# Performance work log

Measured on AMD Instinct MI355X. Metric: run time of the kernel, lower is better.

## Reference

```python
import jax, jax.numpy as jnp
import numpy as np

DIM, HEADS, WS, SHIFT = 192, 6, 8, 4
EPS = 1e-5


def layer_norm(x, g, b):
    mu = jnp.mean(x, axis=-1, keepdims=True)
    var = jnp.mean(jnp.square(x - mu), axis=-1, keepdims=True)
    return (x - mu) * jax.lax.rsqrt(var + EPS) * g + b


def window_partition(x, ws):
    # x: [B, H, W, C] -> [B*nW, ws*ws, C]
    B, H, W, C = x.shape
    x = x.reshape(B, H // ws, ws, W // ws, ws, C)
    return x.transpose(0, 1, 3, 2, 4, 5).reshape(-1, ws * ws, C)


def window_merge(win, ws, B, H, W, C):
    x = win.reshape(B, H // ws, W // ws, ws, ws, C)
    return x.transpose(0, 1, 3, 2, 4, 5).reshape(B, H, W, C)


def make_shift_mask(H, W, ws, shift):
    # standard Swin attention mask for shifted windows (host-side constant)
    img = np.zeros((H, W), dtype=np.float32)
    cnt = 0
    slices = (slice(0, -ws), slice(-ws, -shift), slice(-shift, None))
    for hs in slices:
        for wsl in slices:
            img[hs, wsl] = cnt
            cnt += 1
    m = img.reshape(H // ws, ws, W // ws, ws).transpose(0, 2, 1, 3).reshape(-1, ws * ws)  # [nW, N]
    diff = m[:, None, :] - m[:, :, None]
    return jnp.asarray(np.where(diff != 0, -100.0, 0.0).astype(np.float32))  # [nW, N, N]


def swin_attention(x, qkv_w, qkv_b, proj_w, proj_b, shift):
    B, H, W, C = x.shape
    h, d = HEADS, C // HEADS
    scale = 1.0 / jnp.sqrt(jnp.asarray(d, x.dtype))
    if shift > 0:
        x = jnp.roll(x, shift=(-shift, -shift), axis=(1, 2))
    win = window_partition(x, WS)                       # [Bn, N, C]
    Bn, N, _ = win.shape
    qkv = win @ qkv_w + qkv_b                           # [Bn, N, 3C]
    qkv = qkv.reshape(Bn, N, 3, h, d).transpose(2, 0, 3, 1, 4)
    q, k, v = qkv[0], qkv[1], qkv[2]                    # [Bn, h, N, d]
    attn = jnp.einsum('bhnd,bhmd->bhnm', q, k) * scale  # [Bn, h, N, N]
    if shift > 0:
        mask = make_shift_mask(H, W, WS, shift)         # [nW, N, N]
        nW = mask.shape[0]
        attn = attn.reshape(Bn // nW, nW, h, N, N) + mask[None, :, None]
        attn = attn.reshape(Bn, h, N, N)
    attn = jax.nn.softmax(attn, axis=-1)
    out = jnp.einsum('bhnm,bhmd->bhnd', attn, v)        # [Bn, h, N, d]
    out = out.transpose(0, 2, 1, 3).reshape(Bn, N, C)
    out = out @ proj_w + proj_b
    out = window_merge(out, WS, B, H, W, C)
    if shift > 0:
        out = jnp.roll(out, shift=(shift, shift), axis=(1, 2))
    return out


def setup_inputs() -> dict:
    key = jax.random.key(0)
    ks = jax.random.split(key, 6)
    B, H, W, C = 8, 128, 128, DIM
    s = 0.02
    return {
        'x': jax.random.normal(ks[0], (B, H, W, C), jnp.float32),
        'ln1_g': jnp.ones((C,), jnp.float32),
        'ln1_b': jnp.zeros((C,), jnp.float32),
        'qkv1_w': jax.random.normal(ks[1], (C, 3 * C), jnp.float32) * s,
        'qkv1_b': jnp.zeros((3 * C,), jnp.float32),
        'proj1_w': jax.random.normal(ks[2], (C, C), jnp.float32) * s,
        'proj1_b': jnp.zeros((C,), jnp.float32),
        'ln2_g': jnp.ones((C,), jnp.float32),
        'ln2_b': jnp.zeros((C,), jnp.float32),
        'qkv2_w': jax.random.normal(ks[3], (C, 3 * C), jnp.float32) * s,
        'qkv2_b': jnp.zeros((3 * C,), jnp.float32),
        'proj2_w': jax.random.normal(ks[4], (C, C), jnp.float32) * s,
        'proj2_b': jnp.zeros((C,), jnp.float32),
    }


def reference(x, ln1_g, ln1_b, qkv1_w, qkv1_b, proj1_w, proj1_b,
              ln2_g, ln2_b, qkv2_w, qkv2_b, proj2_w, proj2_b):
    # W-MSA branch (mlp1 is an empty Sequential -> identity)
    y = layer_norm(x, ln1_g, ln1_b)
    x = x + swin_attention(y, qkv1_w, qkv1_b, proj1_w, proj1_b, shift=0)
    # SW-MSA branch (mlp2 is identity)
    y = layer_norm(x, ln2_g, ln2_b)
    x = x + swin_attention(y, qkv2_w, qkv2_b, proj2_w, proj2_b, shift=SHIFT)
    return x
```

## Files before the change

kernel.cpp:

```cpp
#include <hip/hip_runtime.h>

typedef unsigned int   u32;
typedef unsigned short u16;
typedef __bf16 bf16x8 __attribute__((ext_vector_type(8)));
typedef float  f32x4  __attribute__((ext_vector_type(4)));

__device__ __forceinline__ u16 f2bf(float f) {
    u32 u = __builtin_bit_cast(u32, f);
    u += 0x7FFFu + ((u >> 16) & 1u);
    return (u16)(u >> 16);
}
__device__ __forceinline__ u32 pk2bf(float a, float b) {
    return (u32)f2bf(a) | ((u32)f2bf(b) << 16);
}
__device__ __forceinline__ bf16x8 ldfrag(const u16* p) {
    return __builtin_bit_cast(bf16x8, *reinterpret_cast<const uint4*>(p));
}

__device__ __forceinline__ u32 swz(u32 i) { return i ^ ((i >> 3) & 7u); }

template<int SHIFT>
__global__ __launch_bounds__(768) void swin_branch(
    const float* __restrict__ xin, float* __restrict__ xout,
    const float* __restrict__ ln_g, const float* __restrict__ ln_b,
    const u16*   __restrict__ wqkv_t,
    const float* __restrict__ qkv_b,
    const u16*   __restrict__ wproj_t,
    const float* __restrict__ proj_b)
{
    __shared__ __align__(16) u16 smem[49152];
    __shared__ float red1[2][6][64];
    __shared__ float red2[2][6][64];
    constexpr u32 QOFF = 12288;

    const int tid  = threadIdx.x;
    const int win  = (tid >= 384) ? 1 : 0;
    const int lt   = tid - win*384;
    const int wid  = lt >> 6;
    const int lane = lt & 63;
    const int lr   = lane & 15;
    const int lg   = lane >> 4;
    const u32 lsw  = swz((u32)lane);
    const u32 SB   = (u32)win * 24576u;

    const int Wid = blockIdx.x*2 + win;
    const int b   = Wid >> 8;
    const int wy  = (Wid >> 4) & 15;
    const int wx  = Wid & 15;

    {
        const int ty = lane >> 3, tx = lane & 7;
        const int shy = (wy*8 + ty + SHIFT) & 127;
        const int shx = (wx*8 + tx + SHIFT) & 127;
        const float* xp = xin + ((size_t)((b*128 + shy)*128 + shx))*192 + wid*32;
        float xv[32];
        float s1 = 0.f, s2 = 0.f;
        #pragma unroll
        for (int j = 0; j < 8; ++j) {
            float4 v = reinterpret_cast<const float4*>(xp)[j];
            xv[j*4+0]=v.x; xv[j*4+1]=v.y; xv[j*4+2]=v.z; xv[j*4+3]=v.w;
            s1 += v.x+v.y+v.z+v.w;
            s2 += v.x*v.x + v.y*v.y + v.z*v.z + v.w*v.w;
        }
        red1[win][wid][lane] = s1; red2[win][wid][lane] = s2;
        __syncthreads();
        float a1 = 0.f, a2 = 0.f;
        #pragma unroll
        for (int w = 0; w < 6; ++w) { a1 += red1[win][w][lane]; a2 += red2[win][w][lane]; }
        const float mu = a1 * (1.f/192.f);
        const float rs = rsqrtf(a2 * (1.f/192.f) - mu*mu + 1e-5f);
        const float* gp = ln_g + wid*32;
        const float* bp = ln_b + wid*32;
        const u32 yblk = SB + (u32)((lg*6 + wid)*512);
        #pragma unroll
        for (int cc8 = 0; cc8 < 4; ++cc8) {
            u32 pk[4];
            #pragma unroll
            for (int q = 0; q < 4; ++q) {
                int j = cc8*8 + q*2;
                float y0 = (xv[j]   - mu)*rs*gp[j]   + bp[j];
                float y1 = (xv[j+1] - mu)*rs*gp[j+1] + bp[j+1];
                pk[q] = pk2bf(y0, y1);
            }
            *reinterpret_cast<uint4*>(&smem[yblk + swz((u32)(lr + 16*cc8))*8]) =
                make_uint4(pk[0],pk[1],pk[2],pk[3]);
        }
    }
    __syncthreads();

    uint2 kpk[4][2];
    uint2 vpk[4][2];
    {
        {
            f32x4 acc[4][4];
            #pragma unroll
            for (int mi=0; mi<4; ++mi)
                #pragma unroll
                for (int t=0; t<4; ++t) acc[mi][t] = f32x4{0.f,0.f,0.f,0.f};
            #pragma unroll
            for (int ks=0; ks<6; ++ks) {
                bf16x8 af[4];
                #pragma unroll
                for (int mi=0; mi<4; ++mi)
                    af[mi] = ldfrag(&smem[SB + (u32)((mi*6+ks)*512) + lsw*8]);
                bf16x8 bw[4];
                #pragma unroll
                for (int t=0; t<4; ++t)
                    bw[t] = ldfrag(&wqkv_t[((t>>1)*192 + wid*32 + (t&1)*16 + lr)*192 + 32*ks + 8*lg]);
                #pragma unroll
                for (int mi=0; mi<4; ++mi)
                    #pragma unroll
                    for (int t=0; t<4; ++t)
                        acc[mi][t] = __builtin_amdgcn_mfma_f32_16x16x32_bf16(af[mi], bw[t], acc[mi][t], 0,0,0);
            }
            #pragma unroll
            for (int t=0; t<2; ++t) {
                const float bias = qkv_b[wid*32 + t*16 + lr];
                const u32 lphi   = (u32)(16*(2*t + (lr>>3)));
                #pragma unroll
                for (int mi=0; mi<4; ++mi)
                    #pragma unroll
                    for (int rg=0; rg<4; ++rg) {
                        const u32 pos = (u32)(4*lg + rg) + lphi;
                        smem[SB + QOFF + (u32)(wid*2048) + mi*512 + swz(pos)*8 + (lr&7)] =
                            f2bf((acc[mi][t][rg] + bias) * 0.1767766952966369f);
                    }
            }
            #pragma unroll
            for (int t2=0; t2<2; ++t2) {
                const float bias = qkv_b[192 + wid*32 + t2*16 + lr];
                #pragma unroll
                for (int mi=0; mi<4; ++mi)
                    kpk[mi][t2] = make_uint2(
                        pk2bf(acc[mi][2+t2][0] + bias, acc[mi][2+t2][1] + bias),
                        pk2bf(acc[mi][2+t2][2] + bias, acc[mi][2+t2][3] + bias));
            }
        }
        {
            f32x4 vacc[4][2];
            #pragma unroll
            for (int mi=0; mi<4; ++mi)
                #pragma unroll
                for (int t=0; t<2; ++t) vacc[mi][t] = f32x4{0.f,0.f,0.f,0.f};
            #pragma unroll
            for (int ks=0; ks<6; ++ks) {
                bf16x8 af[4];
                #pragma unroll
                for (int mi=0; mi<4; ++mi)
                    af[mi] = ldfrag(&smem[SB + (u32)((mi*6+ks)*512) + lsw*8]);
                bf16x8 bw[2];
                #pragma unroll
                for (int t=0; t<2; ++t)
                    bw[t] = ldfrag(&wqkv_t[(384 + wid*32 + t*16 + lr)*192 + 32*ks + 8*lg]);
                #pragma unroll
                for (int mi=0; mi<4; ++mi)
                    #pragma unroll
                    for (int t=0; t<2; ++t)
                        vacc[mi][t] = __builtin_amdgcn_mfma_f32_16x16x32_bf16(af[mi], bw[t], vacc[mi][t], 0,0,0);
            }
            #pragma unroll
            for (int tv=0; tv<2; ++tv) {
                const float bias = qkv_b[384 + wid*32 + tv*16 + lr];
                #pragma unroll
                for (int mi=0; mi<4; ++mi)
                    vpk[mi][tv] = make_uint2(
                        pk2bf(vacc[mi][tv][0] + bias, vacc[mi][tv][1] + bias),
                        pk2bf(vacc[mi][tv][2] + bias, vacc[mi][tv][3] + bias));
            }
        }
    }
    __syncthreads();

    float rsum[4][4];
    f32x4 o_[4][2];
    {
        const u32 W  = SB + (u32)(wid*512);
        const u32 qb = SB + QOFF + (u32)(wid*2048);
        #define BLK(s) ((u32)(s)*3072u + W)

        #pragma unroll
        for (int t2=0; t2<2; ++t2) {
            const u32 lphi = (u32)(16*(2*t2 + (lr>>3)));
            #pragma unroll
            for (int mi=0; mi<4; ++mi) {
                const u32 a0 = BLK(mi) + (lr&7);
                smem[a0 + swz((u32)(4*lg+0) + lphi)*8] = (u16)(kpk[mi][t2].x);
                smem[a0 + swz((u32)(4*lg+1) + lphi)*8] = (u16)(kpk[mi][t2].x >> 16);
                smem[a0 + swz((u32)(4*lg+2) + lphi)*8] = (u16)(kpk[mi][t2].y);
                smem[a0 + swz((u32)(4*lg+3) + lphi)*8] = (u16)(kpk[mi][t2].y >> 16);
            }
        }
        bf16x8 aq[4], bk[4];
        #pragma unroll
        for (int mi=0; mi<4; ++mi) aq[mi] = ldfrag(&smem[qb + mi*512 + lsw*8]);
        #pragma unroll
        for (int ni=0; ni<4; ++ni) bk[ni] = ldfrag(&smem[BLK(ni) + lsw*8]);
        __builtin_amdgcn_sched_barrier(0);

        #pragma unroll
        for (int tv=0; tv<2; ++tv)
            #pragma unroll
            for (int mi=0; mi<4; ++mi) {
                const u32 pos = (u32)(lr + 16*(2*(mi&1) + (lg>>1)));
                *reinterpret_cast<uint2*>(
                    &smem[BLK(tv*2 + (mi>>1)) + swz(pos)*8 + 4*(lg&1)]) = vpk[mi][tv];
            }

        f32x4 s[4][4];
        #pragma unroll
        for (int mi=0; mi<4; ++mi)
            #pragma unroll
            for (int ni=0; ni<4; ++ni)
                s[mi][ni] = __builtin_amdgcn_mfma_f32_16x16x32_bf16(aq[mi], bk[ni],
                                f32x4{0.f,0.f,0.f,0.f}, 0,0,0);

        if constexpr (SHIFT > 0) {
            int kl[4];
            #pragma unroll
            for (int ni=0; ni<4; ++ni) {
                const int col = 16*ni + lr;
                const int hu = wy*8 + (col>>3);
                const int wu = wx*8 + (col&7);
                kl[ni] = ((hu >= 124) ? 2 : (hu >= 120 ? 1 : 0))*3
                       + ((wu >= 124) ? 2 : (wu >= 120 ? 1 : 0));
            }
            #pragma unroll
            for (int mi=0; mi<4; ++mi)
                #pragma unroll
                for (int rg=0; rg<4; ++rg) {
                    const int row = 16*mi + 4*lg + rg;
                    const int hu = wy*8 + (row>>3);
                    const int wu = wx*8 + (row&7);
                    const int rl = ((hu >= 124) ? 2 : (hu >= 120 ? 1 : 0))*3
                                 + ((wu >= 124) ? 2 : (wu >= 120 ? 1 : 0));
                    #pragma unroll
                    for (int ni=0; ni<4; ++ni)
                        if (rl != kl[ni]) s[mi][ni][rg] += -100.f;
                }
        }

        #pragma unroll
        for (int mi=0; mi<4; ++mi)
            #pragma unroll
            for (int rg=0; rg<4; ++rg) {
                float m = fmaxf(fmaxf(s[mi][0][rg], s[mi][1][rg]), fmaxf(s[mi][2][rg], s[mi][3][rg]));
                #pragma unroll
                for (int off=1; off<16; off<<=1) m = fmaxf(m, __shfl_xor(m, off, 64));
                float sm = 0.f;
                #pragma unroll
                for (int ni=0; ni<4; ++ni) {
                    float e = __expf(s[mi][ni][rg] - m);
                    s[mi][ni][rg] = e;
                    sm += e;
                }
                #pragma unroll
                for (int off=1; off<16; off<<=1) sm += __shfl_xor(sm, off, 64);
                rsum[mi][rg] = 1.0f / sm;
            }

        bf16x8 ap0[4], ap1[4];
        #pragma unroll
        for (int mi=0; mi<4; ++mi)
            #pragma unroll
            for (int ni=0; ni<2; ++ni)
                #pragma unroll
                for (int rg=0; rg<4; ++rg) {
                    const u32 pos = (u32)(4*lg + rg + 16*(2*ni + (lr>>3)));
                    smem[qb + mi*512 + swz(pos)*8 + (lr&7)] = f2bf(s[mi][ni][rg]);
                }
        #pragma unroll
        for (int mi=0; mi<4; ++mi) ap0[mi] = ldfrag(&smem[qb + mi*512 + lsw*8]);
        __builtin_amdgcn_sched_barrier(0);
        #pragma unroll
        for (int mi=0; mi<4; ++mi)
            #pragma unroll
            for (int ni=2; ni<4; ++ni)
                #pragma unroll
                for (int rg=0; rg<4; ++rg) {
                    const u32 pos = (u32)(4*lg + rg + 16*(2*(ni-2) + (lr>>3)));
                    smem[qb + mi*512 + swz(pos)*8 + (lr&7)] = f2bf(s[mi][ni][rg]);
                }
        #pragma unroll
        for (int mi=0; mi<4; ++mi) ap1[mi] = ldfrag(&smem[qb + mi*512 + lsw*8]);
        __builtin_amdgcn_sched_barrier(0);

        bf16x8 bv[2][2];
        #pragma unroll
        for (int tv=0; tv<2; ++tv)
            #pragma unroll
            for (int ksv=0; ksv<2; ++ksv)
                bv[tv][ksv] = ldfrag(&smem[BLK(tv*2+ksv) + lsw*8]);

        #pragma unroll
        for (int mi=0; mi<4; ++mi)
            #pragma unroll
            for (int tv=0; tv<2; ++tv) {
                o_[mi][tv] = __builtin_amdgcn_mfma_f32_16x16x32_bf16(ap0[mi], bv[tv][0],
                                 f32x4{0.f,0.f,0.f,0.f}, 0,0,0);
                o_[mi][tv] = __builtin_amdgcn_mfma_f32_16x16x32_bf16(ap1[mi], bv[tv][1],
                                 o_[mi][tv], 0,0,0);
            }
        __builtin_amdgcn_sched_barrier(0);

        #pragma unroll
        for (int mi=0; mi<4; ++mi)
            #pragma unroll
            for (int tv=0; tv<2; ++tv)
                #pragma unroll
                for (int rg=0; rg<4; ++rg) {
                    const u32 pos = (u32)(4*lg + rg + 16*(2*tv + (lr>>3)));
                    smem[BLK(mi) + swz(pos)*8 + (lr&7)] = f2bf(o_[mi][tv][rg] * rsum[mi][rg]);
                }
        #undef BLK
    }
    __syncthreads();

    {
        f32x4 a2[4][2];
        #pragma unroll
        for (int mi=0; mi<4; ++mi)
            #pragma unroll
            for (int ni=0; ni<2; ++ni) a2[mi][ni] = f32x4{0.f,0.f,0.f,0.f};
        #pragma unroll
        for (int ks=0; ks<6; ++ks) {
            bf16x8 af[4], bw[2];
            #pragma unroll
            for (int mi=0; mi<4; ++mi)
                af[mi] = ldfrag(&smem[SB + (u32)((mi*6+ks)*512) + lsw*8]);
            #pragma unroll
            for (int ni=0; ni<2; ++ni)
                bw[ni] = ldfrag(&wproj_t[(wid*32 + 16*ni + lr)*192 + 32*ks + 8*lg]);
            #pragma unroll
            for (int mi=0; mi<4; ++mi)
                #pragma unroll
                for (int ni=0; ni<2; ++ni)
                    a2[mi][ni] = __builtin_amdgcn_mfma_f32_16x16x32_bf16(af[mi], bw[ni], a2[mi][ni], 0,0,0);
        }
        #pragma unroll
        for (int ni=0; ni<2; ++ni) {
            const int c  = wid*32 + 16*ni + lr;
            const float pb = proj_b[c];
            #pragma unroll
            for (int mi=0; mi<4; ++mi)
                #pragma unroll
                for (int rg=0; rg<4; ++rg) {
                    const int row = 16*mi + 4*lg + rg;
                    const int ty = row >> 3, tx = row & 7;
                    const int shy = (wy*8 + ty + SHIFT) & 127;
                    const int shx = (wx*8 + tx + SHIFT) & 127;
                    const size_t idx = ((size_t)((b*128 + shy)*128 + shx))*192 + c;
                    xout[idx] = xin[idx] + a2[mi][ni][rg] + pb;
                }
        }
    }
}

__global__ void prep_weights(const float* __restrict__ qkv1, const float* __restrict__ proj1,
                             const float* __restrict__ qkv2, const float* __restrict__ proj2,
                             u16* __restrict__ ws)
{
    const int i = blockIdx.x*blockDim.x + threadIdx.x;
    if (i < 110592) {
        const int n = i / 192, k = i - n*192;
        ws[i]          = f2bf(qkv1[k*576 + n]);
        ws[147456 + i] = f2bf(qkv2[k*576 + n]);
    }
    if (i < 36864) {
        const int n = i / 192, k = i - n*192;
        ws[110592 + i] = f2bf(proj1[k*192 + n]);
        ws[258048 + i] = f2bf(proj2[k*192 + n]);
    }
}

extern "C" void kernel_launch(void* const* d_in, const int* in_sizes, int n_in,
                              void* d_out, int out_size, void* d_ws, size_t ws_size,
                              hipStream_t stream)
{
    const float* x       = (const float*)d_in[0];
    const float* ln1_g   = (const float*)d_in[1];
    const float* ln1_b   = (const float*)d_in[2];
    const float* qkv1_w  = (const float*)d_in[3];
    const float* qkv1_b  = (const float*)d_in[4];
    const float* proj1_w = (const float*)d_in[5];
    const float* proj1_b = (const float*)d_in[6];
    const float* ln2_g   = (const float*)d_in[7];
    const float* ln2_b   = (const float*)d_in[8];
    const float* qkv2_w  = (const float*)d_in[9];
    const float* qkv2_b  = (const float*)d_in[10];
    const float* proj2_w = (const float*)d_in[11];
    const float* proj2_b = (const float*)d_in[12];
    float* out = (float*)d_out;
    u16*   wsp = (u16*)d_ws;

    prep_weights<<<dim3(432), dim3(256), 0, stream>>>(qkv1_w, proj1_w, qkv2_w, proj2_w, wsp);
    swin_branch<0><<<dim3(1024), dim3(768), 0, stream>>>(x,   out, ln1_g, ln1_b,
                                                         wsp,        qkv1_b, wsp+110592, proj1_b);
    swin_branch<4><<<dim3(1024), dim3(768), 0, stream>>>(out, out, ln2_g, ln2_b,
                                                         wsp+147456, qkv2_b, wsp+258048, proj2_b);
}
```

Measured before the change: 297.4 us.

## Drop softmax max-subtraction and compute row sums with MFMA against ones

Restructures the attention softmax. Scores are computed one row block at a time and exponentiated directly without subtracting the row max, and shifted-window masking becomes zeroing of masked exponentials instead of adding -100. Row sums now come from MFMA products of the bf16 probabilities with a ones vector, using a fast reciprocal, which removes the cross-lane shuffle reductions for max and sum. Dropping the max subtraction risks overflow if scores are large. Masking by zero also differs slightly from exp(-100), and the sums are taken over bf16-rounded values.

```diff
diff --git a/kernel.cpp b/kernel.cpp
--- a/kernel.cpp
+++ b/kernel.cpp
@@ -137,11 +137,11 @@
             }
         }
         {
-            f32x4 vacc[4][2];
+            f32x4 acc[4][2];
             #pragma unroll
             for (int mi=0; mi<4; ++mi)
                 #pragma unroll
-                for (int t=0; t<2; ++t) vacc[mi][t] = f32x4{0.f,0.f,0.f,0.f};
+                for (int t=0; t<2; ++t) acc[mi][t] = f32x4{0.f,0.f,0.f,0.f};
             #pragma unroll
             for (int ks=0; ks<6; ++ks) {
                 bf16x8 af[4];
@@ -156,7 +156,7 @@
                 for (int mi=0; mi<4; ++mi)
                     #pragma unroll
                     for (int t=0; t<2; ++t)
-                        vacc[mi][t] = __builtin_amdgcn_mfma_f32_16x16x32_bf16(af[mi], bw[t], vacc[mi][t], 0,0,0);
+                        acc[mi][t] = __builtin_amdgcn_mfma_f32_16x16x32_bf16(af[mi], bw[t], acc[mi][t], 0,0,0);
             }
             #pragma unroll
             for (int tv=0; tv<2; ++tv) {
@@ -164,8 +164,8 @@
                 #pragma unroll
                 for (int mi=0; mi<4; ++mi)
                     vpk[mi][tv] = make_uint2(
-                        pk2bf(vacc[mi][tv][0] + bias, vacc[mi][tv][1] + bias),
-                        pk2bf(vacc[mi][tv][2] + bias, vacc[mi][tv][3] + bias));
+                        pk2bf(acc[mi][tv][0] + bias, acc[mi][tv][1] + bias),
+                        pk2bf(acc[mi][tv][2] + bias, acc[mi][tv][3] + bias));
             }
         }
     }
@@ -206,16 +206,8 @@
                     &smem[BLK(tv*2 + (mi>>1)) + swz(pos)*8 + 4*(lg&1)]) = vpk[mi][tv];
             }
 
-        f32x4 s[4][4];
-        #pragma unroll
-        for (int mi=0; mi<4; ++mi)
-            #pragma unroll
-            for (int ni=0; ni<4; ++ni)
-                s[mi][ni] = __builtin_amdgcn_mfma_f32_16x16x32_bf16(aq[mi], bk[ni],
-                                f32x4{0.f,0.f,0.f,0.f}, 0,0,0);
-
+        int kl[4];
         if constexpr (SHIFT > 0) {
-            int kl[4];
             #pragma unroll
             for (int ni=0; ni<4; ++ni) {
                 const int col = 16*ni + lr;
@@ -224,39 +216,39 @@
                 kl[ni] = ((hu >= 124) ? 2 : (hu >= 120 ? 1 : 0))*3
                        + ((wu >= 124) ? 2 : (wu >= 120 ? 1 : 0));
             }
-            #pragma unroll
-            for (int mi=0; mi<4; ++mi)
-                #pragma unroll
-                for (int rg=0; rg<4; ++rg) {
+        }
+        u32 p16[4][4][2];
+        #pragma unroll
+        for (int mi=0; mi<4; ++mi) {
+            f32x4 sr[4];
+            #pragma unroll
+            for (int ni=0; ni<4; ++ni)
+                sr[ni] = __builtin_amdgcn_mfma_f32_16x16x32_bf16(aq[mi], bk[ni],
+                             f32x4{0.f,0.f,0.f,0.f}, 0,0,0);
+            #pragma unroll
+            for (int rg=0; rg<4; ++rg) {
+                int rl = 0;
+                if constexpr (SHIFT > 0) {
                     const int row = 16*mi + 4*lg + rg;
                     const int hu = wy*8 + (row>>3);
                     const int wu = wx*8 + (row&7);
-                    const int rl = ((hu >= 124) ? 2 : (hu >= 120 ? 1 : 0))*3
-                                 + ((wu >= 124) ? 2 : (wu >= 120 ? 1 : 0));
-                    #pragma unroll
-                    for (int ni=0; ni<4; ++ni)
-                        if (rl != kl[ni]) s[mi][ni][rg] += -100.f;
-                }
-        }
-
-        #pragma unroll
-        for (int mi=0; mi<4; ++mi)
-            #pragma unroll
-            for (int rg=0; rg<4; ++rg) {
-                float m = fmaxf(fmaxf(s[mi][0][rg], s[mi][1][rg]), fmaxf(s[mi][2][rg], s[mi][3][rg]));
-                #pragma unroll
-                for (int off=1; off<16; off<<=1) m = fmaxf(m, __shfl_xor(m, off, 64));
-                float sm = 0.f;
+                    rl = ((hu >= 124) ? 2 : (hu >= 120 ? 1 : 0))*3
+                       + ((wu >= 124) ? 2 : (wu >= 120 ? 1 : 0));
+                }
                 #pragma unroll
                 for (int ni=0; ni<4; ++ni) {
-                    float e = __expf(s[mi][ni][rg] - m);
-                    s[mi][ni][rg] = e;
-                    sm += e;
-                }
-                #pragma unroll
-                for (int off=1; off<16; off<<=1) sm += __shfl_xor(sm, off, 64);
-                rsum[mi][rg] = 1.0f / sm;
-            }
+                    float e = __expf(sr[ni][rg]);
+                    if constexpr (SHIFT > 0)
+                        e = (rl == kl[ni]) ? e : 0.f;
+                    sr[ni][rg] = e;
+                }
+            }
+            #pragma unroll
+            for (int ni=0; ni<4; ++ni) {
+                p16[mi][ni][0] = pk2bf(sr[ni][0], sr[ni][1]);
+                p16[mi][ni][1] = pk2bf(sr[ni][2], sr[ni][3]);
+            }
+        }
 
         bf16x8 ap0[4], ap1[4];
         #pragma unroll
@@ -266,7 +258,8 @@
                 #pragma unroll
                 for (int rg=0; rg<4; ++rg) {
                     const u32 pos = (u32)(4*lg + rg + 16*(2*ni + (lr>>3)));
-                    smem[qb + mi*512 + swz(pos)*8 + (lr&7)] = f2bf(s[mi][ni][rg]);
+                    smem[qb + mi*512 + swz(pos)*8 + (lr&7)] =
+                        (u16)(p16[mi][ni][rg>>1] >> (16*(rg&1)));
                 }
         #pragma unroll
         for (int mi=0; mi<4; ++mi) ap0[mi] = ldfrag(&smem[qb + mi*512 + lsw*8]);
@@ -278,11 +271,25 @@
                 #pragma unroll
                 for (int rg=0; rg<4; ++rg) {
                     const u32 pos = (u32)(4*lg + rg + 16*(2*(ni-2) + (lr>>3)));
-                    smem[qb + mi*512 + swz(pos)*8 + (lr&7)] = f2bf(s[mi][ni][rg]);
+                    smem[qb + mi*512 + swz(pos)*8 + (lr&7)] =
+                        (u16)(p16[mi][ni][rg>>1] >> (16*(rg&1)));
                 }
         #pragma unroll
         for (int mi=0; mi<4; ++mi) ap1[mi] = ldfrag(&smem[qb + mi*512 + lsw*8]);
         __builtin_amdgcn_sched_barrier(0);
+
+        bf16x8 vones;
+        #pragma unroll
+        for (int j=0; j<8; ++j) vones[j] = (__bf16)1.0f;
+        #pragma unroll
+        for (int mi=0; mi<4; ++mi) {
+            f32x4 racc = __builtin_amdgcn_mfma_f32_16x16x32_bf16(ap0[mi], vones,
+                             f32x4{0.f,0.f,0.f,0.f}, 0,0,0);
+            racc = __builtin_amdgcn_mfma_f32_16x16x32_bf16(ap1[mi], vones, racc, 0,0,0);
+            #pragma unroll
+            for (int rg=0; rg<4; ++rg)
+                rsum[mi][rg] = __builtin_amdgcn_rcpf(racc[rg]);
+        }
 
         bf16x8 bv[2][2];
         #pragma unroll
```

Result: faster. 268.0 us (-9.9%).
